# Performance work log

Measured on AMD Instinct MI355X. Metric: run time of the kernel, lower is better.

The kernel has to match this reference:

```python
import jax, jax.numpy as jnp
import numpy as np

N_NODES = 100000
N_EDGES = 640000
D_IN = 128
D_OUT = 128

def setup_inputs() -> dict:
    key = jax.random.key(0)
    k1, k2, k3, k4, k5 = jax.random.split(key, 5)
    feat = jax.random.normal(k1, (N_NODES, D_IN), dtype=jnp.float32)
    src = jax.random.randint(k2, (N_EDGES,), 0, N_NODES, dtype=jnp.int32)
    dst = jax.random.randint(k3, (N_EDGES,), 0, N_NODES, dtype=jnp.int32)
    scale = 1.0 / np.sqrt(D_IN)
    W_self = jax.random.normal(k4, (D_IN, D_OUT), dtype=jnp.float32) * scale
    W_neigh = jax.random.normal(k5, (D_IN, D_OUT), dtype=jnp.float32) * scale
    b_self = jnp.zeros((D_OUT,), dtype=jnp.float32)
    b_neigh = jnp.zeros((D_OUT,), dtype=jnp.float32)
    return {"feat": feat, "src": src, "dst": dst,
            "W_self": W_self, "b_self": b_self,
            "W_neigh": W_neigh, "b_neigh": b_neigh}

def reference(feat, src, dst, W_self, b_self, W_neigh, b_neigh):
    # GraphSAGE 'mean' aggregator: copy_src + mean reduce over in-edges, then
    # rst = fc_self(h_self) + fc_neigh(h_neigh). feat_drop=0, no activation/norm.
    n = feat.shape[0]
    msg = feat[src]                                   # [E, D_in] gather
    neigh_sum = jax.ops.segment_sum(msg, dst, num_segments=n)      # [N, D_in]
    deg = jax.ops.segment_sum(jnp.ones_like(dst, dtype=feat.dtype), dst,
                              num_segments=n)          # [N]
    # mean with zero-in-degree nodes -> 0 (DGL semantics)
    h_neigh = neigh_sum / jnp.maximum(deg, 1.0)[:, None]
    rst = feat @ W_self + b_self + h_neigh @ W_neigh + b_neigh      # [N, D_out]
    return rst
```

## Files before the change

kernel.cpp:

```cpp
#include <hip/hip_runtime.h>


constexpr int N_NODES = 100000;
constexpr int N_EDGES = 640000;
constexpr int D = 128;

constexpr int SCAN_ELEMS_PER_BLOCK = 1024;
constexpr int SCAN_NBLOCKS = (N_NODES + SCAN_ELEMS_PER_BLOCK - 1) / SCAN_ELEMS_PER_BLOCK;

typedef __attribute__((ext_vector_type(8))) short bf16x8;
typedef __attribute__((ext_vector_type(4))) float f32x4;

__device__ __forceinline__ unsigned short f2bf(float f) {
    unsigned int u = __float_as_uint(f);
    unsigned int r = u + 0x7FFFu + ((u >> 16) & 1u);
    return (unsigned short)(r >> 16);
}

__global__ __launch_bounds__(256) void zero_deg_kernel(int4* __restrict__ deg4) {
    int i = blockIdx.x * 256 + threadIdx.x;
    if (i < N_NODES / 4) deg4[i] = int4{0, 0, 0, 0};
}

__global__ void prepass_kernel(const int* __restrict__ dst, int* __restrict__ deg,
                               const float* __restrict__ Ws, const float* __restrict__ Wn,
                               unsigned short* __restrict__ wp,
                               const float* __restrict__ feat, unsigned short* __restrict__ fb) {
    const int gid = blockIdx.x * blockDim.x + threadIdx.x;
    if (gid < N_EDGES) atomicAdd(&deg[dst[gid]], 1);
    if (gid < 2 * D * D) {
        int i = gid;
        int r  = i & 7;
        int c  = (i >> 3) & 127;
        int h  = (i >> 10) & 3;
        int ks = (i >> 12) & 3;
        int m  = i >> 14;
        const float* W = m ? Wn : Ws;
        int k = ks * 32 + h * 8 + r;
        wp[i] = f2bf(W[k * D + c]);
    }
    const int total4 = N_NODES * D / 4;
    for (int i = gid; i < total4; i += N_EDGES) {
        float4 v = ((const float4*)feat)[i];
        ushort4 o;
        o.x = f2bf(v.x); o.y = f2bf(v.y); o.z = f2bf(v.z); o.w = f2bf(v.w);
        ((ushort4*)fb)[i] = o;
    }
}


__global__ __launch_bounds__(256) void partial_kernel(const int* __restrict__ deg,
                                                      int* __restrict__ bsum) {
    __shared__ int wsum[4];
    const int tid = threadIdx.x;
    const int base = (blockIdx.x * 256 + tid) * 4;
    int s = 0;
    #pragma unroll
    for (int j = 0; j < 4; j++) {
        int idx = base + j;
        if (idx < N_NODES) s += deg[idx];
    }
    for (int off = 32; off > 0; off >>= 1) s += __shfl_down(s, off, 64);
    if ((tid & 63) == 0) wsum[tid >> 6] = s;
    __syncthreads();
    if (tid == 0) bsum[blockIdx.x] = wsum[0] + wsum[1] + wsum[2] + wsum[3];
}

__global__ __launch_bounds__(128) void scanb_kernel(const int* __restrict__ bsum,
                                                    int* __restrict__ boff,
                                                    int* __restrict__ rowptr) {
    __shared__ int s[128];
    const int tid = threadIdx.x;
    int v = (tid < SCAN_NBLOCKS) ? bsum[tid] : 0;
    s[tid] = v;
    __syncthreads();
    for (int off = 1; off < 128; off <<= 1) {
        int u = (tid >= off) ? s[tid - off] : 0;
        __syncthreads();
        s[tid] += u;
        __syncthreads();
    }
    if (tid < SCAN_NBLOCKS) boff[tid] = s[tid] - v;
    if (tid == 0) rowptr[N_NODES] = N_EDGES;
}

__global__ __launch_bounds__(256) void final_kernel(const int* __restrict__ deg,
                                                    const int* __restrict__ boff,
                                                    int* __restrict__ rowptr,
                                                    int* __restrict__ cursor) {
    __shared__ int wsum[4];
    const int tid = threadIdx.x;
    const int lane = tid & 63;
    const int wave = tid >> 6;
    const int base = (blockIdx.x * 256 + tid) * 4;

    int local[4];
    int tsum = 0;
    #pragma unroll
    for (int j = 0; j < 4; j++) {
        int idx = base + j;
        local[j] = (idx < N_NODES) ? deg[idx] : 0;
        tsum += local[j];
    }
    int incl = tsum;
    for (int off = 1; off < 64; off <<= 1) {
        int u = __shfl_up(incl, off, 64);
        if (lane >= off) incl += u;
    }
    if (lane == 63) wsum[wave] = incl;
    __syncthreads();
    int woff = 0;
    for (int w = 0; w < 4; w++) woff += (w < wave) ? wsum[w] : 0;

    int run = boff[blockIdx.x] + woff + (incl - tsum);
    #pragma unroll
    for (int j = 0; j < 4; j++) {
        int idx = base + j;
        if (idx < N_NODES) {
            rowptr[idx] = run;
            cursor[idx] = run;
            run += local[j];
        }
    }
}

__global__ void fill_kernel(const int* __restrict__ src, const int* __restrict__ dst,
                            int* __restrict__ cursor, int* __restrict__ csr_src) {
    int e = blockIdx.x * blockDim.x + threadIdx.x;
    if (e < N_EDGES) {
        int pos = atomicAdd(&cursor[dst[e]], 1);
        csr_src[pos] = src[e];
    }
}

__global__ __launch_bounds__(256) void gather_kernel(
    const unsigned short* __restrict__ fb, const int* __restrict__ csr_src,
    const int* __restrict__ rowptr, unsigned short* __restrict__ hn)
{
    const int lane = threadIdx.x & 63;
    const int n = (blockIdx.x * blockDim.x + threadIdx.x) >> 6;
    if (n >= N_NODES) return;

    const int e0 = rowptr[n];
    const int e1 = rowptr[n + 1];

    float ax = 0.f, ay = 0.f;
    for (int base = e0; base < e1; base += 8) {
        int sidx[8];
        #pragma unroll
        for (int j = 0; j < 8; j++) {
            int ee = base + j;
            ee = (ee < e1) ? ee : (e1 - 1);
            sidx[j] = csr_src[ee];
        }
        unsigned int v[8];
        #pragma unroll
        for (int j = 0; j < 8; j++)
            v[j] = ((const unsigned int*)(fb + (size_t)sidx[j] * D))[lane];
        #pragma unroll
        for (int j = 0; j < 8; j++) {
            const float w = (base + j < e1) ? 1.0f : 0.0f;
            ax = fmaf(w, __uint_as_float(v[j] << 16), ax);
            ay = fmaf(w, __uint_as_float(v[j] & 0xFFFF0000u), ay);
        }
    }
    const float sc = 1.0f / (float)max(e1 - e0, 1);
    const unsigned int packed =
        ((unsigned int)f2bf(ay * sc) << 16) | (unsigned int)f2bf(ax * sc);
    ((unsigned int*)(hn + (size_t)n * D))[lane] = packed;
}

__global__ __launch_bounds__(256) void mmfused_kernel(
    const unsigned short* __restrict__ fb, const unsigned short* __restrict__ hn,
    const unsigned short* __restrict__ wp,
    const float* __restrict__ b_self, const float* __restrict__ b_neigh,
    float* __restrict__ out)
{
    __shared__ unsigned short lw[2 * 4 * 4 * 128 * 8];

    const int tid = threadIdx.x;
    {
        const uint4* s = (const uint4*)wp;
        uint4* d = (uint4*)lw;
        #pragma unroll
        for (int i = 0; i < 16; i++) d[tid + i * 256] = s[tid + i * 256];
    }
    __syncthreads();

    const int wave = tid >> 6, lane = tid & 63;
    const int h = lane >> 4, c = lane & 15;
    const int row_base = blockIdx.x * 128 + wave * 32;

    bf16x8 a[2][2][4];
    #pragma unroll
    for (int ti = 0; ti < 2; ti++) {
        int row = row_base + ti * 16 + c;
        int rowc = min(row, N_NODES - 1);
        const bf16x8* f0 = (const bf16x8*)(fb + (size_t)rowc * D);
        const bf16x8* f1 = (const bf16x8*)(hn + (size_t)rowc * D);
        #pragma unroll
        for (int ks = 0; ks < 4; ks++) {
            a[0][ti][ks] = f0[ks * 4 + h];
            a[1][ti][ks] = f1[ks * 4 + h];
        }
    }

    for (int ct = 0; ct < 8; ct++) {
        f32x4 acc[2];
        #pragma unroll
        for (int ti = 0; ti < 2; ti++) acc[ti] = f32x4{0.f, 0.f, 0.f, 0.f};

        #pragma unroll
        for (int m = 0; m < 2; m++) {
            bf16x8 b[4];
            #pragma unroll
            for (int ks = 0; ks < 4; ks++)
                b[ks] = ((const bf16x8*)lw)[((m * 4 + ks) * 4 + h) * 128 + ct * 16 + c];
            #pragma unroll
            for (int ks = 0; ks < 4; ks++)
                #pragma unroll
                for (int ti = 0; ti < 2; ti++)
                    acc[ti] = __builtin_amdgcn_mfma_f32_16x16x32_bf16(a[m][ti][ks], b[ks], acc[ti], 0, 0, 0);
        }

        const int col = ct * 16 + c;
        const float bias = b_self[col] + b_neigh[col];
        #pragma unroll
        for (int ti = 0; ti < 2; ti++) {
            if (row_base + ti * 16 < N_NODES) {
                #pragma unroll
                for (int q = 0; q < 4; q++) {
                    int row = row_base + ti * 16 + h * 4 + q;
                    out[(size_t)row * D + col] = acc[ti][q] + bias;
                }
            }
        }
    }
}

extern "C" void kernel_launch(void* const* d_in, const int* in_sizes, int n_in,
                              void* d_out, int out_size, void* d_ws, size_t ws_size,
                              hipStream_t stream) {
    const float* feat    = (const float*)d_in[0];
    const int*   src     = (const int*)d_in[1];
    const int*   dst     = (const int*)d_in[2];
    const float* W_self  = (const float*)d_in[3];
    const float* b_self  = (const float*)d_in[4];
    const float* W_neigh = (const float*)d_in[5];
    const float* b_neigh = (const float*)d_in[6];
    float* out = (float*)d_out;

    unsigned short* fb = (unsigned short*)d_ws;
    unsigned short* hn = fb + (size_t)N_NODES * D;
    unsigned short* wp = hn + (size_t)N_NODES * D;
    int*   deg     = (int*)(wp + 2 * D * D);
    int*   rowptr  = deg + N_NODES;
    int*   cursor  = rowptr + (N_NODES + 1);
    int*   csr_src = cursor + N_NODES;
    int*   bsum    = csr_src + N_EDGES;
    int*   boff    = bsum + SCAN_NBLOCKS;

    zero_deg_kernel<<<(N_NODES / 4 + 255) / 256, 256, 0, stream>>>((int4*)deg);

    prepass_kernel<<<(N_EDGES + 255) / 256, 256, 0, stream>>>(dst, deg, W_self, W_neigh,
                                                              wp, feat, fb);

    partial_kernel<<<SCAN_NBLOCKS, 256, 0, stream>>>(deg, bsum);
    scanb_kernel<<<1, 128, 0, stream>>>(bsum, boff, rowptr);
    final_kernel<<<SCAN_NBLOCKS, 256, 0, stream>>>(deg, boff, rowptr, cursor);

    fill_kernel<<<(N_EDGES + 255) / 256, 256, 0, stream>>>(src, dst, cursor, csr_src);

    gather_kernel<<<25000, 256, 0, stream>>>(fb, csr_src, rowptr, hn);

    mmfused_kernel<<<(N_NODES + 127) / 128, 256, 0, stream>>>(fb, hn, wp, b_self, b_neigh, out);
}
```

Baseline: 137.3 us.

## Fuse neighbor gather into matmul kernel and fold block scan into final pass

The mean-aggregation gather now runs inside the matmul kernel, writing bf16 neighbor means into LDS instead of a global hn buffer. This removes a full write and read of the intermediate. The separate single-block scan kernel is removed; each final_kernel block reduces the preceding block sums itself. In exchange, the gather now runs with far fewer blocks, each wave processing 32 nodes serially. Weight fragments are also read from global/cache instead of LDS, which may reduce latency hiding.

```diff
diff --git a/kernel.cpp b/kernel.cpp
--- a/kernel.cpp
+++ b/kernel.cpp
@@ -66,26 +66,8 @@
     if (tid == 0) bsum[blockIdx.x] = wsum[0] + wsum[1] + wsum[2] + wsum[3];
 }
 
-__global__ __launch_bounds__(128) void scanb_kernel(const int* __restrict__ bsum,
-                                                    int* __restrict__ boff,
-                                                    int* __restrict__ rowptr) {
-    __shared__ int s[128];
-    const int tid = threadIdx.x;
-    int v = (tid < SCAN_NBLOCKS) ? bsum[tid] : 0;
-    s[tid] = v;
-    __syncthreads();
-    for (int off = 1; off < 128; off <<= 1) {
-        int u = (tid >= off) ? s[tid - off] : 0;
-        __syncthreads();
-        s[tid] += u;
-        __syncthreads();
-    }
-    if (tid < SCAN_NBLOCKS) boff[tid] = s[tid] - v;
-    if (tid == 0) rowptr[N_NODES] = N_EDGES;
-}
-
 __global__ __launch_bounds__(256) void final_kernel(const int* __restrict__ deg,
-                                                    const int* __restrict__ boff,
+                                                    const int* __restrict__ bsum,
                                                     int* __restrict__ rowptr,
                                                     int* __restrict__ cursor) {
     __shared__ int wsum[4];
@@ -102,6 +84,14 @@
         local[j] = (idx < N_NODES) ? deg[idx] : 0;
         tsum += local[j];
     }
+
+    int v = (tid < blockIdx.x) ? bsum[tid] : 0;
+    for (int off = 32; off > 0; off >>= 1) v += __shfl_down(v, off, 64);
+    if (lane == 0) wsum[wave] = v;
+    __syncthreads();
+    const int boff = wsum[0] + wsum[1] + wsum[2] + wsum[3];
+    __syncthreads();
+
     int incl = tsum;
     for (int off = 1; off < 64; off <<= 1) {
         int u = __shfl_up(incl, off, 64);
@@ -112,7 +102,7 @@
     int woff = 0;
     for (int w = 0; w < 4; w++) woff += (w < wave) ? wsum[w] : 0;
 
-    int run = boff[blockIdx.x] + woff + (incl - tsum);
+    int run = boff + woff + (incl - tsum);
     #pragma unroll
     for (int j = 0; j < 4; j++) {
         int idx = base + j;
@@ -122,6 +112,7 @@
             run += local[j];
         }
     }
+    if (blockIdx.x == 0 && tid == 0) rowptr[N_NODES] = N_EDGES;
 }
 
 __global__ void fill_kernel(const int* __restrict__ src, const int* __restrict__ dst,
@@ -133,76 +124,69 @@
     }
 }
 
-__global__ __launch_bounds__(256) void gather_kernel(
+__global__ __launch_bounds__(256) void mmgather_kernel(
     const unsigned short* __restrict__ fb, const int* __restrict__ csr_src,
-    const int* __restrict__ rowptr, unsigned short* __restrict__ hn)
-{
-    const int lane = threadIdx.x & 63;
-    const int n = (blockIdx.x * blockDim.x + threadIdx.x) >> 6;
-    if (n >= N_NODES) return;
-
-    const int e0 = rowptr[n];
-    const int e1 = rowptr[n + 1];
-
-    float ax = 0.f, ay = 0.f;
-    for (int base = e0; base < e1; base += 8) {
-        int sidx[8];
-        #pragma unroll
-        for (int j = 0; j < 8; j++) {
-            int ee = base + j;
-            ee = (ee < e1) ? ee : (e1 - 1);
-            sidx[j] = csr_src[ee];
-        }
-        unsigned int v[8];
-        #pragma unroll
-        for (int j = 0; j < 8; j++)
-            v[j] = ((const unsigned int*)(fb + (size_t)sidx[j] * D))[lane];
-        #pragma unroll
-        for (int j = 0; j < 8; j++) {
-            const float w = (base + j < e1) ? 1.0f : 0.0f;
-            ax = fmaf(w, __uint_as_float(v[j] << 16), ax);
-            ay = fmaf(w, __uint_as_float(v[j] & 0xFFFF0000u), ay);
-        }
-    }
-    const float sc = 1.0f / (float)max(e1 - e0, 1);
-    const unsigned int packed =
-        ((unsigned int)f2bf(ay * sc) << 16) | (unsigned int)f2bf(ax * sc);
-    ((unsigned int*)(hn + (size_t)n * D))[lane] = packed;
-}
-
-__global__ __launch_bounds__(256) void mmfused_kernel(
-    const unsigned short* __restrict__ fb, const unsigned short* __restrict__ hn,
-    const unsigned short* __restrict__ wp,
+    const int* __restrict__ rowptr, const unsigned short* __restrict__ wp,
     const float* __restrict__ b_self, const float* __restrict__ b_neigh,
     float* __restrict__ out)
 {
-    __shared__ unsigned short lw[2 * 4 * 4 * 128 * 8];
+    __shared__ unsigned int lhn[128][68];
 
     const int tid = threadIdx.x;
-    {
-        const uint4* s = (const uint4*)wp;
-        uint4* d = (uint4*)lw;
-        #pragma unroll
-        for (int i = 0; i < 16; i++) d[tid + i * 256] = s[tid + i * 256];
-    }
-    __syncthreads();
-
     const int wave = tid >> 6, lane = tid & 63;
+    const int row_base = blockIdx.x * 128;
+
+    for (int i = 0; i < 32; i++) {
+        const int n = row_base + wave * 32 + i;
+        float ax = 0.f, ay = 0.f;
+        float sc = 0.f;
+        if (n < N_NODES) {
+            const int e0 = rowptr[n];
+            const int e1 = rowptr[n + 1];
+            for (int base = e0; base < e1; base += 8) {
+                int sidx[8];
+                #pragma unroll
+                for (int j = 0; j < 8; j++) {
+                    int ee = base + j;
+                    ee = (ee < e1) ? ee : (e1 - 1);
+                    sidx[j] = csr_src[ee];
+                }
+                unsigned int v[8];
+                #pragma unroll
+                for (int j = 0; j < 8; j++)
+                    v[j] = ((const unsigned int*)(fb + (size_t)sidx[j] * D))[lane];
+                #pragma unroll
+                for (int j = 0; j < 8; j++) {
+                    const float w = (base + j < e1) ? 1.0f : 0.0f;
+                    ax = fmaf(w, __uint_as_float(v[j] << 16), ax);
+                    ay = fmaf(w, __uint_as_float(v[j] & 0xFFFF0000u), ay);
+                }
+            }
+            sc = 1.0f / (float)max(e1 - e0, 1);
+        }
+        lhn[wave * 32 + i][lane] =
+            ((unsigned int)f2bf(ay * sc) << 16) | (unsigned int)f2bf(ax * sc);
+    }
+    __syncthreads();
+
     const int h = lane >> 4, c = lane & 15;
-    const int row_base = blockIdx.x * 128 + wave * 32;
-
-    bf16x8 a[2][2][4];
+
+    bf16x8 a0[2][4];
     #pragma unroll
     for (int ti = 0; ti < 2; ti++) {
-        int row = row_base + ti * 16 + c;
+        int row = row_base + wave * 32 + ti * 16 + c;
         int rowc = min(row, N_NODES - 1);
         const bf16x8* f0 = (const bf16x8*)(fb + (size_t)rowc * D);
-        const bf16x8* f1 = (const bf16x8*)(hn + (size_t)rowc * D);
-        #pragma unroll
-        for (int ks = 0; ks < 4; ks++) {
-            a[0][ti][ks] = f0[ks * 4 + h];
-            a[1][ti][ks] = f1[ks * 4 + h];
-        }
+        #pragma unroll
+        for (int ks = 0; ks < 4; ks++) a0[ti][ks] = f0[ks * 4 + h];
+    }
+    bf16x8 a1[2][4];
+    #pragma unroll
+    for (int ti = 0; ti < 2; ti++) {
+        const int lr = wave * 32 + ti * 16 + c;
+        #pragma unroll
+        for (int ks = 0; ks < 4; ks++)
+            a1[ti][ks] = *(const bf16x8*)&lhn[lr][ks * 16 + h * 4];
     }
 
     for (int ct = 0; ct < 8; ct++) {
@@ -211,26 +195,25 @@
         for (int ti = 0; ti < 2; ti++) acc[ti] = f32x4{0.f, 0.f, 0.f, 0.f};
 
         #pragma unroll
-        for (int m = 0; m < 2; m++) {
-            bf16x8 b[4];
+        for (int ks = 0; ks < 4; ks++) {
+            bf16x8 b0 = ((const bf16x8*)wp)[((0 * 4 + ks) * 4 + h) * 128 + ct * 16 + c];
+            bf16x8 b1 = ((const bf16x8*)wp)[((1 * 4 + ks) * 4 + h) * 128 + ct * 16 + c];
             #pragma unroll
-            for (int ks = 0; ks < 4; ks++)
-                b[ks] = ((const bf16x8*)lw)[((m * 4 + ks) * 4 + h) * 128 + ct * 16 + c];
-            #pragma unroll
-            for (int ks = 0; ks < 4; ks++)
-                #pragma unroll
-                for (int ti = 0; ti < 2; ti++)
-                    acc[ti] = __builtin_amdgcn_mfma_f32_16x16x32_bf16(a[m][ti][ks], b[ks], acc[ti], 0, 0, 0);
+            for (int ti = 0; ti < 2; ti++) {
+                acc[ti] = __builtin_amdgcn_mfma_f32_16x16x32_bf16(a0[ti][ks], b0, acc[ti], 0, 0, 0);
+                acc[ti] = __builtin_amdgcn_mfma_f32_16x16x32_bf16(a1[ti][ks], b1, acc[ti], 0, 0, 0);
+            }
         }
 
         const int col = ct * 16 + c;
         const float bias = b_self[col] + b_neigh[col];
         #pragma unroll
         for (int ti = 0; ti < 2; ti++) {
-            if (row_base + ti * 16 < N_NODES) {
+            int tile_row = row_base + wave * 32 + ti * 16;
+            if (tile_row < N_NODES) {
                 #pragma unroll
                 for (int q = 0; q < 4; q++) {
-                    int row = row_base + ti * 16 + h * 4 + q;
+                    int row = tile_row + h * 4 + q;
                     out[(size_t)row * D + col] = acc[ti][q] + bias;
                 }
             }
@@ -251,14 +234,12 @@
     float* out = (float*)d_out;
 
     unsigned short* fb = (unsigned short*)d_ws;
-    unsigned short* hn = fb + (size_t)N_NODES * D;
-    unsigned short* wp = hn + (size_t)N_NODES * D;
+    unsigned short* wp = fb + (size_t)N_NODES * D;
     int*   deg     = (int*)(wp + 2 * D * D);
     int*   rowptr  = deg + N_NODES;
     int*   cursor  = rowptr + (N_NODES + 1);
     int*   csr_src = cursor + N_NODES;
     int*   bsum    = csr_src + N_EDGES;
-    int*   boff    = bsum + SCAN_NBLOCKS;
 
     zero_deg_kernel<<<(N_NODES / 4 + 255) / 256, 256, 0, stream>>>((int4*)deg);
 
@@ -266,12 +247,10 @@
                                                               wp, feat, fb);
 
     partial_kernel<<<SCAN_NBLOCKS, 256, 0, stream>>>(deg, bsum);
-    scanb_kernel<<<1, 128, 0, stream>>>(bsum, boff, rowptr);
-    final_kernel<<<SCAN_NBLOCKS, 256, 0, stream>>>(deg, boff, rowptr, cursor);
+    final_kernel<<<SCAN_NBLOCKS, 256, 0, stream>>>(deg, bsum, rowptr, cursor);
 
     fill_kernel<<<(N_EDGES + 255) / 256, 256, 0, stream>>>(src, dst, cursor, csr_src);
 
-    gather_kernel<<<25000, 256, 0, stream>>>(fb, csr_src, rowptr, hn);
-
-    mmfused_kernel<<<(N_NODES + 127) / 128, 256, 0, stream>>>(fb, hn, wp, b_self, b_neigh, out);
-}
+    mmgather_kernel<<<(N_NODES + 127) / 128, 256, 0, stream>>>(fb, csr_src, rowptr, wp,
+                                                               b_self, b_neigh, out);
+}
```

Result: slower. 143.0 us (+4.1%).
